# Performance work log

Measured on AMD Instinct MI355X. Metric: run time of the kernel, lower is better.

The kernel has to match this reference:

```python
import jax, jax.numpy as jnp
import numpy as np

B, N, K, C = 2, 16384, 16, 128
SHARE = 8
ATTN = C // SHARE  # 16
EPS = 1e-5


def _bn(x, g, b):
    # BatchNorm over all axes except last (channel), training-mode batch stats
    axes = tuple(range(x.ndim - 1))
    m = jnp.mean(x, axis=axes)
    v = jnp.mean(jnp.square(x - m), axis=axes)
    return (x - m) * jax.lax.rsqrt(v + EPS) * g + b


def _index_points(points, idx):
    # points: (B, N, C); idx: (B, N, K) -> (B, N, K, C)
    b, n, k = idx.shape
    flat = idx.reshape(b, n * k, 1)
    out = jnp.take_along_axis(points, flat, axis=1)
    return out.reshape(b, n, k, points.shape[-1])


def setup_inputs() -> dict:
    key = jax.random.key(0)
    ks = jax.random.split(key, 20)
    s = 0.05
    inp = {
        'xyz': jax.random.normal(ks[0], (B, N, 3), jnp.float32),
        'features': jax.random.normal(ks[1], (B, N, C), jnp.float32),
        'knn_idx': jax.random.randint(ks[2], (B, N, K), 0, N, jnp.int32),
        # block params
        'w1': jax.random.normal(ks[3], (C, C), jnp.float32) * s,
        'bn1_g': jnp.ones((C,)), 'bn1_b': jnp.zeros((C,)),
        'lq_w': jax.random.normal(ks[4], (C, C), jnp.float32) * s,
        'lq_b': jnp.zeros((C,)),
        'lk_w': jax.random.normal(ks[5], (C, C), jnp.float32) * s,
        'lk_b': jnp.zeros((C,)),
        'lv_w': jax.random.normal(ks[6], (C, C), jnp.float32) * s,
        'lv_b': jnp.zeros((C,)),
        # fc_delta: Linear(3,3) -> BN(3) -> ReLU -> Linear(3, C)
        'fd_w1': jax.random.normal(ks[7], (3, 3), jnp.float32) * 0.5,
        'fd_b1': jnp.zeros((3,)),
        'fd_bn_g': jnp.ones((3,)), 'fd_bn_b': jnp.zeros((3,)),
        'fd_w2': jax.random.normal(ks[8], (3, C), jnp.float32) * s,
        'fd_b2': jnp.zeros((C,)),
        # fc_gamma: BN(C) -> ReLU -> Linear(C, ATTN) -> BN(ATTN) -> ReLU -> Linear(ATTN, ATTN)
        'fg_bn1_g': jnp.ones((C,)), 'fg_bn1_b': jnp.zeros((C,)),
        'fg_w1': jax.random.normal(ks[9], (C, ATTN), jnp.float32) * s,
        'fg_b1': jnp.zeros((ATTN,)),
        'fg_bn2_g': jnp.ones((ATTN,)), 'fg_bn2_b': jnp.zeros((ATTN,)),
        'fg_w2': jax.random.normal(ks[10], (ATTN, ATTN), jnp.float32) * s,
        'fg_b2': jnp.zeros((ATTN,)),
        'bn2_g': jnp.ones((C,)), 'bn2_b': jnp.zeros((C,)),
        'w3': jax.random.normal(ks[11], (C, C), jnp.float32) * s,
        'bn3_g': jnp.ones((C,)), 'bn3_b': jnp.zeros((C,)),
    }
    return inp


def reference(xyz, features, knn_idx, w1, bn1_g, bn1_b, lq_w, lq_b, lk_w, lk_b,
              lv_w, lv_b, fd_w1, fd_b1, fd_bn_g, fd_bn_b, fd_w2, fd_b2,
              fg_bn1_g, fg_bn1_b, fg_w1, fg_b1, fg_bn2_g, fg_bn2_b, fg_w2, fg_b2,
              bn2_g, bn2_b, w3, bn3_g, bn3_b):
    identity = features
    # linear1 -> bn1 -> relu
    f = jax.nn.relu(_bn(features @ w1, bn1_g, bn1_b))  # (B,N,C)

    # PointTransformerLayer
    q = f @ lq_w + lq_b                          # (B,N,C)
    k = _index_points(f @ lk_w + lk_b, knn_idx)  # (B,N,K,C)
    v = _index_points(f @ lv_w + lv_b, knn_idx)  # (B,N,K,C)
    knn_xyz = _index_points(xyz, knn_idx)        # (B,N,K,3)

    rel = xyz[:, :, None, :] - knn_xyz           # (B,N,K,3)
    pos_enc = jax.nn.relu(_bn(rel @ fd_w1 + fd_b1, fd_bn_g, fd_bn_b)) @ fd_w2 + fd_b2  # (B,N,K,C)

    # einops.reduce 'b n k (s a) -> b n k a' with a=mid_planes=C => s=1, identity sum
    attn = q[:, :, None, :] - k + pos_enc        # (B,N,K,C)
    attn = jax.nn.relu(_bn(attn, fg_bn1_g, fg_bn1_b)) @ fg_w1 + fg_b1   # (B,N,K,ATTN)
    attn = jax.nn.relu(_bn(attn, fg_bn2_g, fg_bn2_b)) @ fg_w2 + fg_b2   # (B,N,K,ATTN)
    attn = jax.nn.softmax(attn, axis=-2)         # softmax over neighbor dim k

    vp = (v + pos_enc).reshape(B, N, K, SHARE, ATTN)
    res = jnp.einsum('bnksa,bnka->bnsa', vp, attn).reshape(B, N, C)

    f2 = jax.nn.relu(_bn(res, bn2_g, bn2_b))
    f3 = _bn(f2 @ w3, bn3_g, bn3_b)
    out = jax.nn.relu(f3 + identity)
    return xyz, out
```

## Files before the change

### kernel.cpp

```cpp
#include <hip/hip_runtime.h>
#include <hip/hip_bf16.h>

constexpr int NPOINTS = 2 * 16384;
constexpr int NSAMP   = NPOINTS * 16;
constexpr int NSLOT   = 64;

constexpr int O_BN1S = 0,     O_BN1Q = 8192;
constexpr int O_FDS  = 16384, O_FDQ  = 16576;
constexpr int O_G1S  = 16768, O_G1Q  = 24960;
constexpr int O_G2S  = 33152, O_G2Q  = 34176;
constexpr int O_BN2S = 35200, O_BN2Q = 43392;
constexpr int O_BN3S = 51584, O_BN3Q = 59776;
constexpr int O_END  = 67968;

typedef __attribute__((ext_vector_type(8))) short short8;
typedef __attribute__((ext_vector_type(4))) short short4v;
typedef __attribute__((ext_vector_type(4))) float f32x4;

__device__ inline unsigned short f2bf(float x) {
    __hip_bfloat16 h = __float2bfloat16(x);
    unsigned short u;
    __builtin_memcpy(&u, &h, 2);
    return u;
}
__device__ inline float bf2f(unsigned short u) {
    return __uint_as_float(((unsigned)u) << 16);
}
__device__ inline float bflo(unsigned u) { return __uint_as_float(u << 16); }
__device__ inline float bfhi(unsigned u) { return __uint_as_float(u & 0xffff0000u); }
__device__ inline unsigned pack2bf(float lo, float hi) {
    float2 f; f.x = lo; f.y = hi;
    __hip_bfloat162 h = __float22bfloat162_rn(f);
    unsigned u; __builtin_memcpy(&u, &h, 4);
    return u;
}

__device__ inline void bn_finalize_block(
    double* dsum, double* dsq, const float* g, const float* b,
    float* scale, float* shift, int nch, double cnt,
    unsigned int* ctr, unsigned int nblk, unsigned int* lastf)
{
    __syncthreads();
    if (threadIdx.x == 0) {
        __threadfence();
        *lastf = (atomicAdd(ctr, 1u) == nblk - 1u) ? 1u : 0u;
    }
    __syncthreads();
    if (*lastf) {
        __threadfence();
        for (int c = threadIdx.x; c < nch; c += blockDim.x) {
            double sm = 0.0, sq = 0.0;
            for (int s = 0; s < NSLOT; ++s) {
                sm += __hip_atomic_load(&dsum[s * nch + c], __ATOMIC_RELAXED, __HIP_MEMORY_SCOPE_AGENT);
                sq += __hip_atomic_load(&dsq[s * nch + c],  __ATOMIC_RELAXED, __HIP_MEMORY_SCOPE_AGENT);
            }
            double m = sm / cnt;
            double v = sq / cnt - m * m;
            double s2 = (double)g[c] / sqrt(v + 1e-5);
            scale[c] = (float)s2;
            shift[c] = (float)((double)b[c] - m * s2);
        }
    }
}

#define PIN_DECODE(x)  const int batch = ((x) >> 2) & 1; \
                       const int qb = (((x) >> 3) << 2) | ((x) & 3);
#define PIN_POINT(s,w) ((batch << 14) + qb * 4 + (w) + ((s) << 12))

#define LOAD_IDX(idx, p) \
    int idx[16]; \
    { const int4* kp_ = (const int4*)(knn + (p) * 16); \
      _Pragma("unroll") \
      for (int q_ = 0; q_ < 4; ++q_) { \
          int4 v_ = kp_[q_]; \
          idx[4*q_+0]=v_.x; idx[4*q_+1]=v_.y; idx[4*q_+2]=v_.z; idx[4*q_+3]=v_.w; } }

template<int ASRC, bool STATS, bool BIAS>
__global__ __launch_bounds__(256) void k_mgemm(
    const void* __restrict__ Ain, const float* __restrict__ W,
    const float* __restrict__ Bias, unsigned short* __restrict__ Out,
    const float* __restrict__ asc, const float* __restrict__ ash,
    double* __restrict__ dsum, double* __restrict__ dsq,
    const float* __restrict__ bng, const float* __restrict__ bnb,
    float* __restrict__ oscale, float* __restrict__ oshift,
    unsigned int* __restrict__ ctr, unsigned int nblk)
{
    __shared__ unsigned short bl[16384];
    __shared__ unsigned int lastf;
    const int tid = threadIdx.x;
    for (int e = tid; e < 16384; e += 256) {
        int k = e >> 7, n = e & 127;
        int f = ((k >> 5) << 2) | ((k >> 3) & 3);
        int dst = f * 1024 + (n >> 4) * 128 + (n & 15) * 8 + (k & 7);
        bl[dst] = f2bf(W[e]);
    }
    __syncthreads();
    const int wid = tid >> 6, lane = tid & 63;
    const int l16 = lane & 15, g = lane >> 4;
    const long arow = (long)blockIdx.x * 64 + wid * 16 + l16;
    short8 afr[4];
    if constexpr (ASRC == 0) {
        const float* A = (const float*)Ain;
        #pragma unroll
        for (int kk = 0; kk < 4; ++kk) {
            const f32x4* src = reinterpret_cast<const f32x4*>(A + arow * 128 + kk * 32 + g * 8);
            f32x4 v0 = src[0], v1 = src[1];
            short8 v;
            #pragma unroll
            for (int i = 0; i < 4; ++i) { v[i] = (short)f2bf(v0[i]); v[4 + i] = (short)f2bf(v1[i]); }
            afr[kk] = v;
        }
    } else if constexpr (ASRC == 1) {
        const unsigned short* A = (const unsigned short*)Ain;
        #pragma unroll
        for (int kk = 0; kk < 4; ++kk)
            afr[kk] = *reinterpret_cast<const short8*>(A + arow * 128 + kk * 32 + g * 8);
    } else {
        const float* A = (const float*)Ain;
        #pragma unroll
        for (int kk = 0; kk < 4; ++kk) {
            const int ch0 = kk * 32 + g * 8;
            const f32x4* src = reinterpret_cast<const f32x4*>(A + arow * 128 + ch0);
            f32x4 v0 = src[0], v1 = src[1];
            short8 v;
            #pragma unroll
            for (int i = 0; i < 4; ++i) {
                v[i]     = (short)f2bf(fmaxf(fmaf(asc[ch0 + i],     v0[i], ash[ch0 + i]),     0.f));
                v[4 + i] = (short)f2bf(fmaxf(fmaf(asc[ch0 + 4 + i], v1[i], ash[ch0 + 4 + i]), 0.f));
            }
            afr[kk] = v;
        }
    }
    f32x4 acc[8];
    #pragma unroll
    for (int n = 0; n < 8; ++n) acc[n] = f32x4{0.f, 0.f, 0.f, 0.f};
    #pragma unroll
    for (int kk = 0; kk < 4; ++kk) {
        const int fb = (kk * 4 + g) * 1024 + l16 * 8;
        #pragma unroll
        for (int n = 0; n < 8; ++n) {
            short8 bf = *reinterpret_cast<const short8*>(&bl[fb + n * 128]);
            acc[n] = __builtin_amdgcn_mfma_f32_16x16x32_bf16(afr[kk], bf, acc[n], 0, 0, 0);
        }
    }
    const long orow0 = (long)blockIdx.x * 64 + wid * 16 + g * 4;
    float bia[8];
    if constexpr (BIAS) {
        #pragma unroll
        for (int n = 0; n < 8; ++n) bia[n] = Bias[n * 16 + l16];
    }
    float lsf[8], lqf[8];
    #pragma unroll
    for (int n = 0; n < 8; ++n) { lsf[n] = 0.f; lqf[n] = 0.f; }
    #pragma unroll
    for (int n = 0; n < 8; ++n) {
        #pragma unroll
        for (int r = 0; r < 4; ++r) {
            float v = acc[n][r];
            if constexpr (BIAS) v += bia[n];
            if constexpr (STATS) { lsf[n] += v; lqf[n] += v * v; }
            Out[(orow0 + r) * 128 + n * 16 + l16] = f2bf(v);
        }
    }
    if constexpr (STATS) {
        const int slot = blockIdx.x & (NSLOT - 1);
        #pragma unroll
        for (int n = 0; n < 8; ++n) {
            float s = lsf[n], q = lqf[n];
            s += __shfl_xor(s, 16); s += __shfl_xor(s, 32);
            q += __shfl_xor(q, 16); q += __shfl_xor(q, 32);
            if (g == 0) {
                atomicAdd(&dsum[slot * 128 + n * 16 + l16], (double)s);
                atomicAdd(&dsq[slot * 128 + n * 16 + l16], (double)q);
            }
        }
        bn_finalize_block(dsum, dsq, bng, bnb, oscale, oshift, 128, (double)NPOINTS, ctr, nblk, &lastf);
    }
}

__global__ __launch_bounds__(512) void k_qkv3(
    const unsigned short* __restrict__ Y,
    const float* __restrict__ sc, const float* __restrict__ sh,
    const float* __restrict__ Wq, const float* __restrict__ Bq,
    const float* __restrict__ Wk, const float* __restrict__ Bk,
    const float* __restrict__ Wv, const float* __restrict__ Bv,
    unsigned short* __restrict__ Qo, unsigned short* __restrict__ Ko,
    unsigned short* __restrict__ Vo)
{
    __shared__ unsigned short bl[3 * 16384];
    const int tid = threadIdx.x;
    #pragma unroll
    for (int m = 0; m < 3; ++m) {
        const float* W = (m == 0) ? Wq : (m == 1) ? Wk : Wv;
        for (int e = tid; e < 16384; e += 512) {
            int k = e >> 7, n = e & 127;
            int f = ((k >> 5) << 2) | ((k >> 3) & 3);
            bl[m * 16384 + f * 1024 + (n >> 4) * 128 + (n & 15) * 8 + (k & 7)] = f2bf(W[e]);
        }
    }
    __syncthreads();
    const int wid = tid >> 6, lane = tid & 63;
    const int l16 = lane & 15, g = lane >> 4;
    const long arow = (long)blockIdx.x * 128 + wid * 16 + l16;
    short8 afr[4];
    #pragma unroll
    for (int kk = 0; kk < 4; ++kk) {
        const int ch0 = kk * 32 + g * 8;
        short8 raw = *reinterpret_cast<const short8*>(Y + arow * 128 + ch0);
        short8 v;
        #pragma unroll
        for (int i = 0; i < 8; ++i) {
            float x = fmaxf(fmaf(sc[ch0 + i], bf2f((unsigned short)raw[i]), sh[ch0 + i]), 0.f);
            v[i] = (short)f2bf(x);
        }
        afr[kk] = v;
    }
    const long orow0 = (long)blockIdx.x * 128 + wid * 16 + g * 4;
    #pragma unroll
    for (int m = 0; m < 3; ++m) {
        const float* Bias = (m == 0) ? Bq : (m == 1) ? Bk : Bv;
        unsigned short* Out = (m == 0) ? Qo : (m == 1) ? Ko : Vo;
        f32x4 acc[8];
        #pragma unroll
        for (int n = 0; n < 8; ++n) acc[n] = f32x4{0.f, 0.f, 0.f, 0.f};
        #pragma unroll
        for (int kk = 0; kk < 4; ++kk) {
            const int fb = m * 16384 + (kk * 4 + g) * 1024 + l16 * 8;
            #pragma unroll
            for (int n = 0; n < 8; ++n) {
                short8 bf = *reinterpret_cast<const short8*>(&bl[fb + n * 128]);
                acc[n] = __builtin_amdgcn_mfma_f32_16x16x32_bf16(afr[kk], bf, acc[n], 0, 0, 0);
            }
        }
        #pragma unroll
        for (int n = 0; n < 8; ++n) {
            const float bia = Bias[n * 16 + l16];
            #pragma unroll
            for (int r = 0; r < 4; ++r)
                Out[(orow0 + r) * 128 + n * 16 + l16] = f2bf(acc[n][r] + bia);
        }
    }
}

__global__ __launch_bounds__(256) void k_fd_stats(
    const float* __restrict__ xyz, const int* __restrict__ knn,
    const float* __restrict__ fdw1, const float* __restrict__ fdb1,
    double* __restrict__ dsum, double* __restrict__ dsq,
    const float* __restrict__ bng, const float* __restrict__ bnb,
    float* __restrict__ oscale, float* __restrict__ oshift,
    unsigned int* __restrict__ ctr, unsigned int nblk)
{
    __shared__ unsigned int lastf;
    float wd[9], bd[3];
    #pragma unroll
    for (int i = 0; i < 9; ++i) wd[i] = fdw1[i];
    #pragma unroll
    for (int j = 0; j < 3; ++j) bd[j] = fdb1[j];
    double ls[3] = {0, 0, 0}, lq[3] = {0, 0, 0};
    for (int s = blockIdx.x * blockDim.x + threadIdx.x; s < NSAMP; s += gridDim.x * blockDim.x) {
        int p = s >> 4;
        int b = p >> 14, n = p & 16383;
        int idx = knn[s];
        const float* pa = xyz + (b * 16384 + n) * 3;
        const float* pb = xyz + (b * 16384 + idx) * 3;
        float r0 = pa[0] - pb[0], r1 = pa[1] - pb[1], r2 = pa[2] - pb[2];
        #pragma unroll
        for (int j = 0; j < 3; ++j) {
            float h = r0 * wd[j] + r1 * wd[3 + j] + r2 * wd[6 + j] + bd[j];
            ls[j] += h; lq[j] += (double)h * h;
        }
    }
    const int slot = blockIdx.x & (NSLOT - 1);
    #pragma unroll
    for (int j = 0; j < 3; ++j) {
        double v = ls[j];
        for (int o = 32; o; o >>= 1) v += __shfl_down(v, o);
        if ((threadIdx.x & 63) == 0) atomicAdd(&dsum[slot * 3 + j], v);
        v = lq[j];
        for (int o = 32; o; o >>= 1) v += __shfl_down(v, o);
        if ((threadIdx.x & 63) == 0) atomicAdd(&dsq[slot * 3 + j], v);
    }
    bn_finalize_block(dsum, dsq, bng, bnb, oscale, oshift, 3, (double)NSAMP, ctr, nblk, &lastf);
}

__global__ __launch_bounds__(256) void k_attn1_stats(
    const unsigned short* __restrict__ Q, const unsigned short* __restrict__ Kb,
    const float* __restrict__ xyz, const int* __restrict__ knn,
    const float* __restrict__ fdw1, const float* __restrict__ fdb1,
    const float* __restrict__ fds, const float* __restrict__ fdh,
    const float* __restrict__ fdw2, const float* __restrict__ fdb2,
    double* __restrict__ dsum, double* __restrict__ dsq,
    const float* __restrict__ bng, const float* __restrict__ bnb,
    float* __restrict__ oscale, float* __restrict__ oshift,
    unsigned int* __restrict__ ctr, unsigned int nblk)
{
    __shared__ float pe3_all[4][16][4];
    __shared__ double red[1024];
    __shared__ unsigned int lastf;
    const int tid = threadIdx.x, w = tid >> 6, l = tid & 63;
    float (*pe3)[4] = pe3_all[w];
    const int c0 = 2 * l;
    const float w0a = fdw2[c0],       w0b = fdw2[c0 + 1];
    const float w1a = fdw2[128 + c0], w1b = fdw2[129 + c0];
    const float w2a = fdw2[256 + c0], w2b = fdw2[257 + c0];
    const float bba = fdb2[c0],       bbb = fdb2[c0 + 1];
    float wd[9], bd[3], fs3[3], fh3[3];
    #pragma unroll
    for (int i = 0; i < 9; ++i) wd[i] = fdw1[i];
    #pragma unroll
    for (int j = 0; j < 3; ++j) { bd[j] = fdb1[j]; fs3[j] = fds[j]; fh3[j] = fdh[j]; }
    PIN_DECODE(blockIdx.x);
    const unsigned* kb32 = (const unsigned*)(Kb + (((size_t)batch) << 14) * 128);
    double ls0 = 0, lq0 = 0, ls1 = 0, lq1 = 0;
    for (int s = 0; s < 4; ++s) {
        const int p = PIN_POINT(s, w);
        LOAD_IDX(idx, p);
        if (l < 16) {
            const int mi = knn[p * 16 + l];
            const int n = p & 16383;
            const float* pa = xyz + (batch * 16384 + n) * 3;
            const float* pb = xyz + (batch * 16384 + mi) * 3;
            const float r0 = pa[0] - pb[0], r1 = pa[1] - pb[1], r2 = pa[2] - pb[2];
            #pragma unroll
            for (int j = 0; j < 3; ++j) {
                float h = r0 * wd[j] + r1 * wd[3 + j] + r2 * wd[6 + j] + bd[j];
                pe3[l][j] = fmaxf(fmaf(fs3[j], h, fh3[j]), 0.f);
            }
        }
        unsigned kw[16];
        #pragma unroll
        for (int kk = 0; kk < 16; ++kk) kw[kk] = kb32[idx[kk] * 64 + l];
        const unsigned qw = ((const unsigned*)(Q + (size_t)p * 128))[l];
        const float qa = bflo(qw), qb = bfhi(qw);
        float pls0 = 0.f, plq0 = 0.f, pls1 = 0.f, plq1 = 0.f;
        #pragma unroll
        for (int kk = 0; kk < 16; ++kk) {
            const float pea = fmaf(pe3[kk][0], w0a, fmaf(pe3[kk][1], w1a, fmaf(pe3[kk][2], w2a, bba)));
            const float peb = fmaf(pe3[kk][0], w0b, fmaf(pe3[kk][1], w1b, fmaf(pe3[kk][2], w2b, bbb)));
            const float a0 = qa - bflo(kw[kk]) + pea;
            const float a1 = qb - bfhi(kw[kk]) + peb;
            pls0 += a0; plq0 = fmaf(a0, a0, plq0);
            pls1 += a1; plq1 = fmaf(a1, a1, plq1);
        }
        ls0 += pls0; lq0 += plq0; ls1 += pls1; lq1 += plq1;
    }
    red[tid] = ls0; red[256 + tid] = ls1; red[512 + tid] = lq0; red[768 + tid] = lq1;
    __syncthreads();
    if (w == 0) {
        const int slot = blockIdx.x & (NSLOT - 1);
        const double s0 = red[l] + red[64 + l] + red[128 + l] + red[192 + l];
        const double s1 = red[256 + l] + red[320 + l] + red[384 + l] + red[448 + l];
        const double q0 = red[512 + l] + red[576 + l] + red[640 + l] + red[704 + l];
        const double q1 = red[768 + l] + red[832 + l] + red[896 + l] + red[960 + l];
        atomicAdd(&dsum[slot * 128 + c0], s0); atomicAdd(&dsum[slot * 128 + c0 + 1], s1);
        atomicAdd(&dsq[slot * 128 + c0], q0); atomicAdd(&dsq[slot * 128 + c0 + 1], q1);
    }
    bn_finalize_block(dsum, dsq, bng, bnb, oscale, oshift, 128, (double)NSAMP, ctr, nblk, &lastf);
}

__global__ __launch_bounds__(256) void k_attn2_stats(
    const unsigned short* __restrict__ Q, const unsigned short* __restrict__ Kb,
    const float* __restrict__ xyz, const int* __restrict__ knn,
    const float* __restrict__ fdw1, const float* __restrict__ fdb1,
    const float* __restrict__ fds, const float* __restrict__ fdh,
    const float* __restrict__ fdw2, const float* __restrict__ fdb2,
    const float* __restrict__ g1s, const float* __restrict__ g1h,
    const float* __restrict__ fgw1, const float* __restrict__ fgb1,
    unsigned short* __restrict__ Tb,
    double* __restrict__ dsum, double* __restrict__ dsq,
    const float* __restrict__ bng, const float* __restrict__ bnb,
    float* __restrict__ oscale, float* __restrict__ oshift,
    unsigned int* __restrict__ ctr, unsigned int nblk)
{
    __shared__ __align__(16) unsigned short s1b_all[4][2048];
    __shared__ float pe3_all[4][16][4];
    __shared__ unsigned int lastf;
    const int tid = threadIdx.x, w = tid >> 6, l = tid & 63;
    unsigned short* s1b = s1b_all[w];
    float (*pe3)[4] = pe3_all[w];
    const int c0 = 2 * l;
    const int a16 = l & 15, g8 = (l >> 4) * 8;
    const float w0a = fdw2[c0],       w0b = fdw2[c0 + 1];
    const float w1a = fdw2[128 + c0], w1b = fdw2[129 + c0];
    const float w2a = fdw2[256 + c0], w2b = fdw2[257 + c0];
    const float bba = fdb2[c0],       bbb = fdb2[c0 + 1];
    const float sA = g1s[c0], hA = g1h[c0];
    const float sB = g1s[c0 + 1], hB = g1h[c0 + 1];
    const float tb = fgb1[a16];
    float wd[9], bd[3], fs3[3], fh3[3];
    #pragma unroll
    for (int i = 0; i < 9; ++i) wd[i] = fdw1[i];
    #pragma unroll
    for (int j = 0; j < 3; ++j) { bd[j] = fdb1[j]; fs3[j] = fds[j]; fh3[j] = fdh[j]; }
    short8 bfrag[4];
    #pragma unroll
    for (int s = 0; s < 4; ++s)
        #pragma unroll
        for (int i = 0; i < 8; ++i)
            bfrag[s][i] = (short)f2bf(fgw1[(32 * s + g8 + i) * 16 + a16]);
    PIN_DECODE(blockIdx.x);
    const unsigned* kb32 = (const unsigned*)(Kb + (((size_t)batch) << 14) * 128);
    double ls = 0.0, lq = 0.0;
    for (int s = 0; s < 4; ++s) {
        const int p = PIN_POINT(s, w);
        LOAD_IDX(idx, p);
        if (l < 16) {
            const int mi = knn[p * 16 + l];
            const int n = p & 16383;
            const float* pa = xyz + (batch * 16384 + n) * 3;
            const float* pb = xyz + (batch * 16384 + mi) * 3;
            const float r0 = pa[0] - pb[0], r1 = pa[1] - pb[1], r2 = pa[2] - pb[2];
            #pragma unroll
            for (int j = 0; j < 3; ++j) {
                float h = r0 * wd[j] + r1 * wd[3 + j] + r2 * wd[6 + j] + bd[j];
                pe3[l][j] = fmaxf(fmaf(fs3[j], h, fh3[j]), 0.f);
            }
        }
        unsigned kw[16];
        #pragma unroll
        for (int kk = 0; kk < 16; ++kk) kw[kk] = kb32[idx[kk] * 64 + l];
        const unsigned qw = ((const unsigned*)(Q + (size_t)p * 128))[l];
        const float qa = bflo(qw), qb = bfhi(qw);
        #pragma unroll
        for (int kk = 0; kk < 16; ++kk) {
            const float pea = fmaf(pe3[kk][0], w0a, fmaf(pe3[kk][1], w1a, fmaf(pe3[kk][2], w2a, bba)));
            const float peb = fmaf(pe3[kk][0], w0b, fmaf(pe3[kk][1], w1b, fmaf(pe3[kk][2], w2b, bbb)));
            const float a0 = qa - bflo(kw[kk]) + pea;
            const float a1 = qb - bfhi(kw[kk]) + peb;
            const float v0 = fmaxf(fmaf(sA, a0, hA), 0.f);
            const float v1 = fmaxf(fmaf(sB, a1, hB), 0.f);
            ((unsigned*)s1b)[(((kk * 128 + c0) ^ ((kk & 7) << 3)) >> 1)] = pack2bf(v0, v1);
        }
        f32x4 acc = {0.f, 0.f, 0.f, 0.f};
        #pragma unroll
        for (int ss = 0; ss < 4; ++ss) {
            const int ai = (a16 * 128 + ss * 32 + g8) ^ ((a16 & 7) << 3);
            short8 af = *reinterpret_cast<const short8*>(&s1b[ai]);
            acc = __builtin_amdgcn_mfma_f32_16x16x32_bf16(af, bfrag[ss], acc, 0, 0, 0);
        }
        short4v tq;
        float pls = 0.f, plq = 0.f;
        #pragma unroll
        for (int r = 0; r < 4; ++r) {
            const float t = acc[r] + tb;
            tq[r] = (short)f2bf(t);
            pls += t; plq = fmaf(t, t, plq);
        }
        *reinterpret_cast<short4v*>(Tb + (size_t)p * 256 + l * 4) = tq;
        ls += pls; lq += plq;
    }
    __syncthreads();
    double* red = (double*)&s1b_all[0][0];
    red[tid] = ls; red[256 + tid] = lq;
    __syncthreads();
    if (tid < 16) {
        const int slot = blockIdx.x & (NSLOT - 1);
        double s = 0.0, q = 0.0;
        for (int i = 0; i < 16; ++i) { s += red[tid + 16 * i]; q += red[256 + tid + 16 * i]; }
        atomicAdd(&dsum[slot * 16 + tid], s); atomicAdd(&dsq[slot * 16 + tid], q);
    }
    bn_finalize_block(dsum, dsq, bng, bnb, oscale, oshift, 16, (double)NSAMP, ctr, nblk, &lastf);
}

__global__ __launch_bounds__(256) void k_attn_final(
    const unsigned short* __restrict__ Tb, const unsigned short* __restrict__ Vb,
    const float* __restrict__ xyz, const int* __restrict__ knn,
    const float* __restrict__ fdw1, const float* __restrict__ fdb1,
    const float* __restrict__ fds, const float* __restrict__ fdh,
    const float* __restrict__ fdw2, const float* __restrict__ fdb2,
    const float* __restrict__ g2s, const float* __restrict__ g2h,
    const float* __restrict__ fgw2, const float* __restrict__ fgb2,
    float* __restrict__ Res, double* __restrict__ dsum, double* __restrict__ dsq,
    const float* __restrict__ bng, const float* __restrict__ bnb,
    float* __restrict__ oscale, float* __restrict__ oshift,
    unsigned int* __restrict__ ctr, unsigned int nblk)
{
    __shared__ float t2l_all[4][272];
    __shared__ float wl_all[4][272];
    __shared__ float pe3_all[4][16][4];
    __shared__ double red[1024];
    __shared__ unsigned int lastf;
    const int tid = threadIdx.x, w = tid >> 6, l = tid & 63;
    float* t2l = t2l_all[w];
    float* wl  = wl_all[w];
    float (*pe3)[4] = pe3_all[w];
    const int c0 = 2 * l;
    const int a16 = l & 15, g4 = l >> 4;
    const int aA = c0 & 15;
    const float w0a = fdw2[c0],       w0b = fdw2[c0 + 1];
    const float w1a = fdw2[128 + c0], w1b = fdw2[129 + c0];
    const float w2a = fdw2[256 + c0], w2b = fdw2[257 + c0];
    const float bba = fdb2[c0],       bbb = fdb2[c0 + 1];
    const float s2a = g2s[a16], s2h = g2h[a16], b2a = fgb2[a16];
    float wd[9], bd[3], fs3[3], fh3[3];
    #pragma unroll
    for (int i = 0; i < 9; ++i) wd[i] = fdw1[i];
    #pragma unroll
    for (int j = 0; j < 3; ++j) { bd[j] = fdb1[j]; fs3[j] = fds[j]; fh3[j] = fdh[j]; }
    float wv2[16];
    #pragma unroll
    for (int j = 0; j < 16; ++j) wv2[j] = fgw2[j * 16 + a16];
    PIN_DECODE(blockIdx.x);
    const unsigned* vb32 = (const unsigned*)(Vb + (((size_t)batch) << 14) * 128);
    double lsA = 0.0, lqA = 0.0, lsB = 0.0, lqB = 0.0;
    for (int s = 0; s < 4; ++s) {
        const int p = PIN_POINT(s, w);
        LOAD_IDX(idx, p);
        unsigned vw[16];
        #pragma unroll
        for (int kk = 0; kk < 16; ++kk) vw[kk] = vb32[idx[kk] * 64 + l];
        if (l < 16) {
            const int mi = knn[p * 16 + l];
            const int n = p & 16383;
            const float* pa = xyz + (batch * 16384 + n) * 3;
            const float* pb = xyz + (batch * 16384 + mi) * 3;
            const float r0 = pa[0] - pb[0], r1 = pa[1] - pb[1], r2 = pa[2] - pb[2];
            #pragma unroll
            for (int j = 0; j < 3; ++j) {
                float h = r0 * wd[j] + r1 * wd[3 + j] + r2 * wd[6 + j] + bd[j];
                pe3[l][j] = fmaxf(fmaf(fs3[j], h, fh3[j]), 0.f);
            }
        }
        short4v tv = *reinterpret_cast<const short4v*>(Tb + (size_t)p * 256 + l * 4);
        #pragma unroll
        for (int r = 0; r < 4; ++r)
            t2l[(g4 * 4 + r) * 17 + a16] = fmaxf(fmaf(s2a, bf2f((unsigned short)tv[r]), s2h), 0.f);
        float ur[4];
        #pragma unroll
        for (int r = 0; r < 4; ++r) {
            float u = b2a;
            #pragma unroll
            for (int j = 0; j < 16; ++j) u = fmaf(t2l[(g4 * 4 + r) * 17 + j], wv2[j], u);
            ur[r] = u;
        }
        float m = fmaxf(fmaxf(ur[0], ur[1]), fmaxf(ur[2], ur[3]));
        m = fmaxf(m, __shfl_xor(m, 16));
        m = fmaxf(m, __shfl_xor(m, 32));
        const float e0 = __expf(ur[0] - m), e1 = __expf(ur[1] - m);
        const float e2 = __expf(ur[2] - m), e3 = __expf(ur[3] - m);
        float ss = e0 + e1 + e2 + e3;
        ss += __shfl_xor(ss, 16);
        ss += __shfl_xor(ss, 32);
        const float inv = 1.f / ss;
        wl[(g4 * 4 + 0) * 17 + a16] = e0 * inv;
        wl[(g4 * 4 + 1) * 17 + a16] = e1 * inv;
        wl[(g4 * 4 + 2) * 17 + a16] = e2 * inv;
        wl[(g4 * 4 + 3) * 17 + a16] = e3 * inv;
        float rc0 = 0.f, rc1 = 0.f;
        #pragma unroll
        for (int kk = 0; kk < 16; ++kk) {
            const float wgtA = wl[kk * 17 + aA];
            const float wgtB = wl[kk * 17 + aA + 1];
            const float pea = fmaf(pe3[kk][0], w0a, fmaf(pe3[kk][1], w1a, fmaf(pe3[kk][2], w2a, bba)));
            const float peb = fmaf(pe3[kk][0], w0b, fmaf(pe3[kk][1], w1b, fmaf(pe3[kk][2], w2b, bbb)));
            rc0 = fmaf(bflo(vw[kk]) + pea, wgtA, rc0);
            rc1 = fmaf(bfhi(vw[kk]) + peb, wgtB, rc1);
        }
        float2 rcv; rcv.x = rc0; rcv.y = rc1;
        *reinterpret_cast<float2*>(Res + (size_t)p * 128 + c0) = rcv;
        lsA += rc0; lqA += (double)rc0 * rc0;
        lsB += rc1; lqB += (double)rc1 * rc1;
    }
    red[tid] = lsA; red[256 + tid] = lsB; red[512 + tid] = lqA; red[768 + tid] = lqB;
    __syncthreads();
    if (w == 0) {
        const int slot = blockIdx.x & (NSLOT - 1);
        const double s0 = red[l] + red[64 + l] + red[128 + l] + red[192 + l];
        const double s1 = red[256 + l] + red[320 + l] + red[384 + l] + red[448 + l];
        const double q0 = red[512 + l] + red[576 + l] + red[640 + l] + red[704 + l];
        const double q1 = red[768 + l] + red[832 + l] + red[896 + l] + red[960 + l];
        atomicAdd(&dsum[slot * 128 + c0], s0); atomicAdd(&dsum[slot * 128 + c0 + 1], s1);
        atomicAdd(&dsq[slot * 128 + c0], q0); atomicAdd(&dsq[slot * 128 + c0 + 1], q1);
    }
    bn_finalize_block(dsum, dsq, bng, bnb, oscale, oshift, 128, (double)NPOINTS, ctr, nblk, &lastf);
}

__global__ __launch_bounds__(256) void k_out(
    const unsigned short* __restrict__ Y3, const float* __restrict__ sc,
    const float* __restrict__ sh, const float* __restrict__ feat,
    float* __restrict__ out)
{
    const int v = blockIdx.x * blockDim.x + threadIdx.x;
    const int base = v * 8;
    short8 y = *reinterpret_cast<const short8*>(&Y3[base]);
    const int c0 = base & 127;
    #pragma unroll
    for (int j = 0; j < 8; ++j) {
        float val = fmaf(sc[c0 + j], bf2f((unsigned short)y[j]), sh[c0 + j]) + feat[base + j];
        out[base + j] = fmaxf(val, 0.f);
    }
}

__global__ void k_copy_f32(const float* __restrict__ s, float* __restrict__ d, int n)
{
    for (int i = blockIdx.x * blockDim.x + threadIdx.x; i < n; i += gridDim.x * blockDim.x) d[i] = s[i];
}

extern "C" void kernel_launch(void* const* d_in, const int* in_sizes, int n_in,
                              void* d_out, int out_size, void* d_ws, size_t ws_size,
                              hipStream_t stream)
{
    (void)in_sizes; (void)n_in; (void)out_size; (void)ws_size;
    const float* xyz   = (const float*)d_in[0];
    const float* feat  = (const float*)d_in[1];
    const int*   knn   = (const int*)d_in[2];
    const float* w1    = (const float*)d_in[3];
    const float* bn1g  = (const float*)d_in[4];
    const float* bn1b  = (const float*)d_in[5];
    const float* lqw   = (const float*)d_in[6];
    const float* lqb   = (const float*)d_in[7];
    const float* lkw   = (const float*)d_in[8];
    const float* lkb   = (const float*)d_in[9];
    const float* lvw   = (const float*)d_in[10];
    const float* lvb   = (const float*)d_in[11];
    const float* fdw1  = (const float*)d_in[12];
    const float* fdb1  = (const float*)d_in[13];
    const float* fdbng = (const float*)d_in[14];
    const float* fdbnb = (const float*)d_in[15];
    const float* fdw2  = (const float*)d_in[16];
    const float* fdb2  = (const float*)d_in[17];
    const float* g1g   = (const float*)d_in[18];
    const float* g1b   = (const float*)d_in[19];
    const float* fgw1  = (const float*)d_in[20];
    const float* fgb1  = (const float*)d_in[21];
    const float* g2g   = (const float*)d_in[22];
    const float* g2b   = (const float*)d_in[23];
    const float* fgw2  = (const float*)d_in[24];
    const float* fgb2  = (const float*)d_in[25];
    const float* bn2g  = (const float*)d_in[26];
    const float* bn2b  = (const float*)d_in[27];
    const float* w3    = (const float*)d_in[28];
    const float* bn3g  = (const float*)d_in[29];
    const float* bn3b  = (const float*)d_in[30];

    unsigned short* YBF = (unsigned short*)d_ws;
    float*          RES = (float*)d_ws;
    unsigned short* Qb  = YBF + 2 * 4194304;
    unsigned short* Kb  = Qb + 4194304;
    unsigned short* Vb  = Kb + 4194304;
    unsigned short* Tb  = Vb + 4194304;
    unsigned short* Y3  = Qb;
    double* ds = (double*)(Tb + 8388608);
    unsigned int* ctrs = (unsigned int*)(ds + O_END);
    float* fs = (float*)(ds + O_END + 8);

    hipMemsetAsync(ds, 0, (size_t)(O_END + 8) * sizeof(double), stream);

    k_mgemm<0, true, false><<<512, 256, 0, stream>>>(feat, w1, nullptr, YBF, nullptr, nullptr,
                                                     ds + O_BN1S, ds + O_BN1Q,
                                                     bn1g, bn1b, fs + 0, fs + 128, ctrs + 0, 512u);
    k_qkv3<<<256, 512, 0, stream>>>(YBF, fs + 0, fs + 128, lqw, lqb, lkw, lkb, lvw, lvb, Qb, Kb, Vb);
    k_fd_stats<<<256, 256, 0, stream>>>(xyz, knn, fdw1, fdb1, ds + O_FDS, ds + O_FDQ,
                                        fdbng, fdbnb, fs + 256, fs + 264, ctrs + 1, 256u);
    k_attn1_stats<<<2048, 256, 0, stream>>>(Qb, Kb, xyz, knn, fdw1, fdb1, fs + 256, fs + 264,
                                            fdw2, fdb2, ds + O_G1S, ds + O_G1Q,
                                            g1g, g1b, fs + 272, fs + 400, ctrs + 2, 2048u);
    k_attn2_stats<<<2048, 256, 0, stream>>>(Qb, Kb, xyz, knn, fdw1, fdb1, fs + 256, fs + 264,
                                            fdw2, fdb2, fs + 272, fs + 400, fgw1, fgb1, Tb,
                                            ds + O_G2S, ds + O_G2Q,
                                            g2g, g2b, fs + 528, fs + 544, ctrs + 3, 2048u);
    k_attn_final<<<2048, 256, 0, stream>>>(Tb, Vb, xyz, knn, fdw1, fdb1, fs + 256, fs + 264,
                                           fdw2, fdb2, fs + 528, fs + 544, fgw2, fgb2,
                                           RES, ds + O_BN2S, ds + O_BN2Q,
                                           bn2g, bn2b, fs + 560, fs + 688, ctrs + 4, 2048u);
    k_mgemm<2, true, false><<<512, 256, 0, stream>>>(RES, w3, nullptr, Y3, fs + 560, fs + 688,
                                                     ds + O_BN3S, ds + O_BN3Q,
                                                     bn3g, bn3b, fs + 816, fs + 944, ctrs + 5, 512u);
    float* outp = (float*)d_out;
    k_out<<<2048, 256, 0, stream>>>(Y3, fs + 816, fs + 944, feat, outp + 98304);
    k_copy_f32<<<192, 256, 0, stream>>>(xyz, outp, 98304);
}
```

Before: 359.6 us.

## Batch two points per wave in attention kernels and store result in bf16

The three attention kernels now handle 2 points per wave instead of 4 sequential ones. They issue all index and neighbor gathers for both points up front to raise memory-level parallelism, and the grid doubles to 4096 blocks. The attention result buffer is now stored as bf16 instead of fp32, with a new GEMM input mode that converts it back, halving that intermediate's traffic. This adds register pressure from holding 32 gathered words, more blocks doing atomic stat reductions, and lower precision on the residual before BN2.

```diff
diff --git a/kernel.cpp b/kernel.cpp
--- a/kernel.cpp
+++ b/kernel.cpp
@@ -65,15 +65,7 @@
 
 #define PIN_DECODE(x)  const int batch = ((x) >> 2) & 1; \
                        const int qb = (((x) >> 3) << 2) | ((x) & 3);
-#define PIN_POINT(s,w) ((batch << 14) + qb * 4 + (w) + ((s) << 12))
-
-#define LOAD_IDX(idx, p) \
-    int idx[16]; \
-    { const int4* kp_ = (const int4*)(knn + (p) * 16); \
-      _Pragma("unroll") \
-      for (int q_ = 0; q_ < 4; ++q_) { \
-          int4 v_ = kp_[q_]; \
-          idx[4*q_+0]=v_.x; idx[4*q_+1]=v_.y; idx[4*q_+2]=v_.z; idx[4*q_+3]=v_.w; } }
+#define PIN_PT(s,w)    ((batch << 14) + qb * 4 + (w) + ((s) << 13))
 
 template<int ASRC, bool STATS, bool BIAS>
 __global__ __launch_bounds__(256) void k_mgemm(
@@ -115,7 +107,7 @@
         #pragma unroll
         for (int kk = 0; kk < 4; ++kk)
             afr[kk] = *reinterpret_cast<const short8*>(A + arow * 128 + kk * 32 + g * 8);
-    } else {
+    } else if constexpr (ASRC == 2) {
         const float* A = (const float*)Ain;
         #pragma unroll
         for (int kk = 0; kk < 4; ++kk) {
@@ -127,6 +119,20 @@
             for (int i = 0; i < 4; ++i) {
                 v[i]     = (short)f2bf(fmaxf(fmaf(asc[ch0 + i],     v0[i], ash[ch0 + i]),     0.f));
                 v[4 + i] = (short)f2bf(fmaxf(fmaf(asc[ch0 + 4 + i], v1[i], ash[ch0 + 4 + i]), 0.f));
+            }
+            afr[kk] = v;
+        }
+    } else {
+        const unsigned short* A = (const unsigned short*)Ain;
+        #pragma unroll
+        for (int kk = 0; kk < 4; ++kk) {
+            const int ch0 = kk * 32 + g * 8;
+            short8 raw = *reinterpret_cast<const short8*>(A + arow * 128 + ch0);
+            short8 v;
+            #pragma unroll
+            for (int i = 0; i < 8; ++i) {
+                float x = fmaxf(fmaf(asc[ch0 + i], bf2f((unsigned short)raw[i]), ash[ch0 + i]), 0.f);
+                v[i] = (short)f2bf(x);
             }
             afr[kk] = v;
         }
@@ -294,11 +300,11 @@
     float* __restrict__ oscale, float* __restrict__ oshift,
     unsigned int* __restrict__ ctr, unsigned int nblk)
 {
-    __shared__ float pe3_all[4][16][4];
+    __shared__ float pe3_all[4][2][16][4];
     __shared__ double red[1024];
     __shared__ unsigned int lastf;
     const int tid = threadIdx.x, w = tid >> 6, l = tid & 63;
-    float (*pe3)[4] = pe3_all[w];
+    float (*pe3)[16][4] = pe3_all[w];
     const int c0 = 2 * l;
     const float w0a = fdw2[c0],       w0b = fdw2[c0 + 1];
     const float w1a = fdw2[128 + c0], w1b = fdw2[129 + c0];
@@ -311,34 +317,51 @@
     for (int j = 0; j < 3; ++j) { bd[j] = fdb1[j]; fs3[j] = fds[j]; fh3[j] = fdh[j]; }
     PIN_DECODE(blockIdx.x);
     const unsigned* kb32 = (const unsigned*)(Kb + (((size_t)batch) << 14) * 128);
-    double ls0 = 0, lq0 = 0, ls1 = 0, lq1 = 0;
-    for (int s = 0; s < 4; ++s) {
-        const int p = PIN_POINT(s, w);
-        LOAD_IDX(idx, p);
-        if (l < 16) {
-            const int mi = knn[p * 16 + l];
-            const int n = p & 16383;
+    const int pts[2] = {PIN_PT(0, w), PIN_PT(1, w)};
+    int idx[2][16];
+    #pragma unroll
+    for (int t = 0; t < 2; ++t) {
+        const int4* kp = (const int4*)(knn + (size_t)pts[t] * 16);
+        #pragma unroll
+        for (int q = 0; q < 4; ++q) {
+            int4 v = kp[q];
+            idx[t][4 * q] = v.x; idx[t][4 * q + 1] = v.y; idx[t][4 * q + 2] = v.z; idx[t][4 * q + 3] = v.w;
+        }
+    }
+    unsigned kw[2][16];
+    #pragma unroll
+    for (int t = 0; t < 2; ++t)
+        #pragma unroll
+        for (int kk = 0; kk < 16; ++kk) kw[t][kk] = kb32[idx[t][kk] * 64 + l];
+    unsigned qw[2];
+    #pragma unroll
+    for (int t = 0; t < 2; ++t) qw[t] = ((const unsigned*)(Q + (size_t)pts[t] * 128))[l];
+    if (l < 16) {
+        #pragma unroll
+        for (int t = 0; t < 2; ++t) {
+            const int mi = knn[pts[t] * 16 + l];
+            const int n = pts[t] & 16383;
             const float* pa = xyz + (batch * 16384 + n) * 3;
             const float* pb = xyz + (batch * 16384 + mi) * 3;
             const float r0 = pa[0] - pb[0], r1 = pa[1] - pb[1], r2 = pa[2] - pb[2];
             #pragma unroll
             for (int j = 0; j < 3; ++j) {
                 float h = r0 * wd[j] + r1 * wd[3 + j] + r2 * wd[6 + j] + bd[j];
-                pe3[l][j] = fmaxf(fmaf(fs3[j], h, fh3[j]), 0.f);
+                pe3[t][l][j] = fmaxf(fmaf(fs3[j], h, fh3[j]), 0.f);
             }
         }
-        unsigned kw[16];
-        #pragma unroll
-        for (int kk = 0; kk < 16; ++kk) kw[kk] = kb32[idx[kk] * 64 + l];
-        const unsigned qw = ((const unsigned*)(Q + (size_t)p * 128))[l];
-        const float qa = bflo(qw), qb = bfhi(qw);
+    }
+    double ls0 = 0, lq0 = 0, ls1 = 0, lq1 = 0;
+    #pragma unroll
+    for (int t = 0; t < 2; ++t) {
+        const float qa = bflo(qw[t]), qb = bfhi(qw[t]);
         float pls0 = 0.f, plq0 = 0.f, pls1 = 0.f, plq1 = 0.f;
         #pragma unroll
         for (int kk = 0; kk < 16; ++kk) {
-            const float pea = fmaf(pe3[kk][0], w0a, fmaf(pe3[kk][1], w1a, fmaf(pe3[kk][2], w2a, bba)));
-            const float peb = fmaf(pe3[kk][0], w0b, fmaf(pe3[kk][1], w1b, fmaf(pe3[kk][2], w2b, bbb)));
-            const float a0 = qa - bflo(kw[kk]) + pea;
-            const float a1 = qb - bfhi(kw[kk]) + peb;
+            const float pea = fmaf(pe3[t][kk][0], w0a, fmaf(pe3[t][kk][1], w1a, fmaf(pe3[t][kk][2], w2a, bba)));
+            const float peb = fmaf(pe3[t][kk][0], w0b, fmaf(pe3[t][kk][1], w1b, fmaf(pe3[t][kk][2], w2b, bbb)));
+            const float a0 = qa - bflo(kw[t][kk]) + pea;
+            const float a1 = qb - bfhi(kw[t][kk]) + peb;
             pls0 += a0; plq0 = fmaf(a0, a0, plq0);
             pls1 += a1; plq1 = fmaf(a1, a1, plq1);
         }
@@ -373,11 +396,11 @@
     unsigned int* __restrict__ ctr, unsigned int nblk)
 {
     __shared__ __align__(16) unsigned short s1b_all[4][2048];
-    __shared__ float pe3_all[4][16][4];
+    __shared__ float pe3_all[4][2][16][4];
     __shared__ unsigned int lastf;
     const int tid = threadIdx.x, w = tid >> 6, l = tid & 63;
     unsigned short* s1b = s1b_all[w];
-    float (*pe3)[4] = pe3_all[w];
+    float (*pe3)[16][4] = pe3_all[w];
     const int c0 = 2 * l;
     const int a16 = l & 15, g8 = (l >> 4) * 8;
     const float w0a = fdw2[c0],       w0b = fdw2[c0 + 1];
@@ -400,33 +423,50 @@
             bfrag[s][i] = (short)f2bf(fgw1[(32 * s + g8 + i) * 16 + a16]);
     PIN_DECODE(blockIdx.x);
     const unsigned* kb32 = (const unsigned*)(Kb + (((size_t)batch) << 14) * 128);
-    double ls = 0.0, lq = 0.0;
-    for (int s = 0; s < 4; ++s) {
-        const int p = PIN_POINT(s, w);
-        LOAD_IDX(idx, p);
-        if (l < 16) {
-            const int mi = knn[p * 16 + l];
-            const int n = p & 16383;
+    const int pts[2] = {PIN_PT(0, w), PIN_PT(1, w)};
+    int idx[2][16];
+    #pragma unroll
+    for (int t = 0; t < 2; ++t) {
+        const int4* kp = (const int4*)(knn + (size_t)pts[t] * 16);
+        #pragma unroll
+        for (int q = 0; q < 4; ++q) {
+            int4 v = kp[q];
+            idx[t][4 * q] = v.x; idx[t][4 * q + 1] = v.y; idx[t][4 * q + 2] = v.z; idx[t][4 * q + 3] = v.w;
+        }
+    }
+    unsigned kw[2][16];
+    #pragma unroll
+    for (int t = 0; t < 2; ++t)
+        #pragma unroll
+        for (int kk = 0; kk < 16; ++kk) kw[t][kk] = kb32[idx[t][kk] * 64 + l];
+    unsigned qw[2];
+    #pragma unroll
+    for (int t = 0; t < 2; ++t) qw[t] = ((const unsigned*)(Q + (size_t)pts[t] * 128))[l];
+    if (l < 16) {
+        #pragma unroll
+        for (int t = 0; t < 2; ++t) {
+            const int mi = knn[pts[t] * 16 + l];
+            const int n = pts[t] & 16383;
             const float* pa = xyz + (batch * 16384 + n) * 3;
             const float* pb = xyz + (batch * 16384 + mi) * 3;
             const float r0 = pa[0] - pb[0], r1 = pa[1] - pb[1], r2 = pa[2] - pb[2];
             #pragma unroll
             for (int j = 0; j < 3; ++j) {
                 float h = r0 * wd[j] + r1 * wd[3 + j] + r2 * wd[6 + j] + bd[j];
-                pe3[l][j] = fmaxf(fmaf(fs3[j], h, fh3[j]), 0.f);
+                pe3[t][l][j] = fmaxf(fmaf(fs3[j], h, fh3[j]), 0.f);
             }
         }
-        unsigned kw[16];
-        #pragma unroll
-        for (int kk = 0; kk < 16; ++kk) kw[kk] = kb32[idx[kk] * 64 + l];
-        const unsigned qw = ((const unsigned*)(Q + (size_t)p * 128))[l];
-        const float qa = bflo(qw), qb = bfhi(qw);
+    }
+    double ls = 0.0, lq = 0.0;
+    #pragma unroll
+    for (int t = 0; t < 2; ++t) {
+        const float qa = bflo(qw[t]), qb = bfhi(qw[t]);
         #pragma unroll
         for (int kk = 0; kk < 16; ++kk) {
-            const float pea = fmaf(pe3[kk][0], w0a, fmaf(pe3[kk][1], w1a, fmaf(pe3[kk][2], w2a, bba)));
-            const float peb = fmaf(pe3[kk][0], w0b, fmaf(pe3[kk][1], w1b, fmaf(pe3[kk][2], w2b, bbb)));
-            const float a0 = qa - bflo(kw[kk]) + pea;
-            const float a1 = qb - bfhi(kw[kk]) + peb;
+            const float pea = fmaf(pe3[t][kk][0], w0a, fmaf(pe3[t][kk][1], w1a, fmaf(pe3[t][kk][2], w2a, bba)));
+            const float peb = fmaf(pe3[t][kk][0], w0b, fmaf(pe3[t][kk][1], w1b, fmaf(pe3[t][kk][2], w2b, bbb)));
+            const float a0 = qa - bflo(kw[t][kk]) + pea;
+            const float a1 = qb - bfhi(kw[t][kk]) + peb;
             const float v0 = fmaxf(fmaf(sA, a0, hA), 0.f);
             const float v1 = fmaxf(fmaf(sB, a1, hB), 0.f);
             ((unsigned*)s1b)[(((kk * 128 + c0) ^ ((kk & 7) << 3)) >> 1)] = pack2bf(v0, v1);
@@ -442,11 +482,11 @@
         float pls = 0.f, plq = 0.f;
         #pragma unroll
         for (int r = 0; r < 4; ++r) {
-            const float t = acc[r] + tb;
-            tq[r] = (short)f2bf(t);
-            pls += t; plq = fmaf(t, t, plq);
-        }
-        *reinterpret_cast<short4v*>(Tb + (size_t)p * 256 + l * 4) = tq;
+            const float tt = acc[r] + tb;
+            tq[r] = (short)f2bf(tt);
+            pls += tt; plq = fmaf(tt, tt, plq);
+        }
+        *reinterpret_cast<short4v*>(Tb + (size_t)pts[t] * 256 + l * 4) = tq;
         ls += pls; lq += plq;
     }
     __syncthreads();
@@ -470,20 +510,20 @@
     const float* __restrict__ fdw2, const float* __restrict__ fdb2,
     const float* __restrict__ g2s, const float* __restrict__ g2h,
     const float* __restrict__ fgw2, const float* __restrict__ fgb2,
-    float* __restrict__ Res, double* __restrict__ dsum, double* __restrict__ dsq,
+    unsigned short* __restrict__ Res, double* __restrict__ dsum, double* __restrict__ dsq,
     const float* __restrict__ bng, const float* __restrict__ bnb,
     float* __restrict__ oscale, float* __restrict__ oshift,
     unsigned int* __restrict__ ctr, unsigned int nblk)
 {
     __shared__ float t2l_all[4][272];
     __shared__ float wl_all[4][272];
-    __shared__ float pe3_all[4][16][4];
+    __shared__ float pe3_all[4][2][16][4];
     __shared__ double red[1024];
     __shared__ unsigned int lastf;
     const int tid = threadIdx.x, w = tid >> 6, l = tid & 63;
     float* t2l = t2l_all[w];
     float* wl  = wl_all[w];
-    float (*pe3)[4] = pe3_all[w];
+    float (*pe3)[16][4] = pe3_all[w];
     const int c0 = 2 * l;
     const int a16 = l & 15, g4 = l >> 4;
     const int aA = c0 & 15;
@@ -502,29 +542,47 @@
     for (int j = 0; j < 16; ++j) wv2[j] = fgw2[j * 16 + a16];
     PIN_DECODE(blockIdx.x);
     const unsigned* vb32 = (const unsigned*)(Vb + (((size_t)batch) << 14) * 128);
-    double lsA = 0.0, lqA = 0.0, lsB = 0.0, lqB = 0.0;
-    for (int s = 0; s < 4; ++s) {
-        const int p = PIN_POINT(s, w);
-        LOAD_IDX(idx, p);
-        unsigned vw[16];
-        #pragma unroll
-        for (int kk = 0; kk < 16; ++kk) vw[kk] = vb32[idx[kk] * 64 + l];
-        if (l < 16) {
-            const int mi = knn[p * 16 + l];
-            const int n = p & 16383;
+    const int pts[2] = {PIN_PT(0, w), PIN_PT(1, w)};
+    int idx[2][16];
+    #pragma unroll
+    for (int t = 0; t < 2; ++t) {
+        const int4* kp = (const int4*)(knn + (size_t)pts[t] * 16);
+        #pragma unroll
+        for (int q = 0; q < 4; ++q) {
+            int4 v = kp[q];
+            idx[t][4 * q] = v.x; idx[t][4 * q + 1] = v.y; idx[t][4 * q + 2] = v.z; idx[t][4 * q + 3] = v.w;
+        }
+    }
+    unsigned vw[2][16];
+    #pragma unroll
+    for (int t = 0; t < 2; ++t)
+        #pragma unroll
+        for (int kk = 0; kk < 16; ++kk) vw[t][kk] = vb32[idx[t][kk] * 64 + l];
+    short4v tv[2];
+    #pragma unroll
+    for (int t = 0; t < 2; ++t)
+        tv[t] = *reinterpret_cast<const short4v*>(Tb + (size_t)pts[t] * 256 + l * 4);
+    if (l < 16) {
+        #pragma unroll
+        for (int t = 0; t < 2; ++t) {
+            const int mi = knn[pts[t] * 16 + l];
+            const int n = pts[t] & 16383;
             const float* pa = xyz + (batch * 16384 + n) * 3;
             const float* pb = xyz + (batch * 16384 + mi) * 3;
             const float r0 = pa[0] - pb[0], r1 = pa[1] - pb[1], r2 = pa[2] - pb[2];
             #pragma unroll
             for (int j = 0; j < 3; ++j) {
                 float h = r0 * wd[j] + r1 * wd[3 + j] + r2 * wd[6 + j] + bd[j];
-                pe3[l][j] = fmaxf(fmaf(fs3[j], h, fh3[j]), 0.f);
+                pe3[t][l][j] = fmaxf(fmaf(fs3[j], h, fh3[j]), 0.f);
             }
         }
-        short4v tv = *reinterpret_cast<const short4v*>(Tb + (size_t)p * 256 + l * 4);
+    }
+    double lsA = 0.0, lqA = 0.0, lsB = 0.0, lqB = 0.0;
+    #pragma unroll
+    for (int t = 0; t < 2; ++t) {
         #pragma unroll
         for (int r = 0; r < 4; ++r)
-            t2l[(g4 * 4 + r) * 17 + a16] = fmaxf(fmaf(s2a, bf2f((unsigned short)tv[r]), s2h), 0.f);
+            t2l[(g4 * 4 + r) * 17 + a16] = fmaxf(fmaf(s2a, bf2f((unsigned short)tv[t][r]), s2h), 0.f);
         float ur[4];
         #pragma unroll
         for (int r = 0; r < 4; ++r) {
@@ -551,15 +609,14 @@
         for (int kk = 0; kk < 16; ++kk) {
             const float wgtA = wl[kk * 17 + aA];
             const float wgtB = wl[kk * 17 + aA + 1];
-            const float pea = fmaf(pe3[kk][0], w0a, fmaf(pe3[kk][1], w1a, fmaf(pe3[kk][2], w2a, bba)));
-            const float peb = fmaf(pe3[kk][0], w0b, fmaf(pe3[kk][1], w1b, fmaf(pe3[kk][2], w2b, bbb)));
-            rc0 = fmaf(bflo(vw[kk]) + pea, wgtA, rc0);
-            rc1 = fmaf(bfhi(vw[kk]) + peb, wgtB, rc1);
-        }
-        float2 rcv; rcv.x = rc0; rcv.y = rc1;
-        *reinterpret_cast<float2*>(Res + (size_t)p * 128 + c0) = rcv;
-        lsA += rc0; lqA += (double)rc0 * rc0;
-        lsB += rc1; lqB += (double)rc1 * rc1;
+            const float pea = fmaf(pe3[t][kk][0], w0a, fmaf(pe3[t][kk][1], w1a, fmaf(pe3[t][kk][2], w2a, bba)));
+            const float peb = fmaf(pe3[t][kk][0], w0b, fmaf(pe3[t][kk][1], w1b, fmaf(pe3[t][kk][2], w2b, bbb)));
+            rc0 = fmaf(bflo(vw[t][kk]) + pea, wgtA, rc0);
+            rc1 = fmaf(bfhi(vw[t][kk]) + peb, wgtB, rc1);
+        }
+        ((unsigned*)Res)[(size_t)pts[t] * 64 + l] = pack2bf(rc0, rc1);
+        if (t == 0) { lsA += rc0; lqA += (double)rc0 * rc0; lsB += rc1; lqB += (double)rc1 * rc1; }
+        else        { lsA += rc0; lqA += (double)rc0 * rc0; lsB += rc1; lqB += (double)rc1 * rc1; }
     }
     red[tid] = lsA; red[256 + tid] = lsB; red[512 + tid] = lqA; red[768 + tid] = lqB;
     __syncthreads();
@@ -634,7 +691,7 @@
     const float* bn3b  = (const float*)d_in[30];
 
     unsigned short* YBF = (unsigned short*)d_ws;
-    float*          RES = (float*)d_ws;
+    unsigned short* RES = YBF;
     unsigned short* Qb  = YBF + 2 * 4194304;
     unsigned short* Kb  = Qb + 4194304;
     unsigned short* Vb  = Kb + 4194304;
@@ -652,18 +709,18 @@
     k_qkv3<<<256, 512, 0, stream>>>(YBF, fs + 0, fs + 128, lqw, lqb, lkw, lkb, lvw, lvb, Qb, Kb, Vb);
     k_fd_stats<<<256, 256, 0, stream>>>(xyz, knn, fdw1, fdb1, ds + O_FDS, ds + O_FDQ,
                                         fdbng, fdbnb, fs + 256, fs + 264, ctrs + 1, 256u);
-    k_attn1_stats<<<2048, 256, 0, stream>>>(Qb, Kb, xyz, knn, fdw1, fdb1, fs + 256, fs + 264,
+    k_attn1_stats<<<4096, 256, 0, stream>>>(Qb, Kb, xyz, knn, fdw1, fdb1, fs + 256, fs + 264,
                                             fdw2, fdb2, ds + O_G1S, ds + O_G1Q,
-                                            g1g, g1b, fs + 272, fs + 400, ctrs + 2, 2048u);
-    k_attn2_stats<<<2048, 256, 0, stream>>>(Qb, Kb, xyz, knn, fdw1, fdb1, fs + 256, fs + 264,
+                                            g1g, g1b, fs + 272, fs + 400, ctrs + 2, 4096u);
+    k_attn2_stats<<<4096, 256, 0, stream>>>(Qb, Kb, xyz, knn, fdw1, fdb1, fs + 256, fs + 264,
                                             fdw2, fdb2, fs + 272, fs + 400, fgw1, fgb1, Tb,
                                             ds + O_G2S, ds + O_G2Q,
-                                            g2g, g2b, fs + 528, fs + 544, ctrs + 3, 2048u);
-    k_attn_final<<<2048, 256, 0, stream>>>(Tb, Vb, xyz, knn, fdw1, fdb1, fs + 256, fs + 264,
+                                            g2g, g2b, fs + 528, fs + 544, ctrs + 3, 4096u);
+    k_attn_final<<<4096, 256, 0, stream>>>(Tb, Vb, xyz, knn, fdw1, fdb1, fs + 256, fs + 264,
                                            fdw2, fdb2, fs + 528, fs + 544, fgw2, fgb2,
                                            RES, ds + O_BN2S, ds + O_BN2Q,
-                                           bn2g, bn2b, fs + 560, fs + 688, ctrs + 4, 2048u);
-    k_mgemm<2, true, false><<<512, 256, 0, stream>>>(RES, w3, nullptr, Y3, fs + 560, fs + 688,
+                                           bn2g, bn2b, fs + 560, fs + 688, ctrs + 4, 4096u);
+    k_mgemm<3, true, false><<<512, 256, 0, stream>>>(RES, w3, nullptr, Y3, fs + 560, fs + 688,
                                                      ds + O_BN3S, ds + O_BN3Q,
                                                      bn3g, bn3b, fs + 816, fs + 944, ctrs + 5, 512u);
     float* outp = (float*)d_out;
```

Measured after the change: 507.3 us. +41.1%, slower.
